# Performance work log

Measured on AMD Instinct MI355X. Metric: run time of the kernel, lower is better.

The kernel has to match this reference:

```python
import jax, jax.numpy as jnp
import numpy as np

B, N, QD = 4, 4096, 1024
HEADS, DIM_HEAD = 8, 64
HID = HEADS * DIM_HEAD
SCALE = DIM_HEAD ** -0.5


def setup_inputs() -> dict:
    key = jax.random.key(0)
    ks = jax.random.split(key, 6)
    s_in = 1.0 / np.sqrt(QD)
    s_h = 1.0 / np.sqrt(HID)
    return {
        "x": jax.random.normal(ks[0], (B, N, QD), dtype=jnp.float32),
        "Wq": jax.random.uniform(ks[1], (QD, HID), jnp.float32, -s_in, s_in),
        "Wk": jax.random.uniform(ks[2], (QD, HID), jnp.float32, -s_in, s_in),
        "Wv": jax.random.uniform(ks[3], (QD, HID), jnp.float32, -s_in, s_in),
        "Wo": jax.random.uniform(ks[4], (HID, QD), jnp.float32, -s_h, s_h),
        "bo": jax.random.uniform(ks[5], (QD,), jnp.float32, -s_h, s_h),
    }


def reference(x, Wq, Wk, Wv, Wo, bo):
    b, n, _ = x.shape
    # projections (bias-free Linears)
    q = x @ Wq  # [b, n, hid]
    k = x @ Wk
    v = x @ Wv
    # 'b n (h d) -> b h d n'
    def split_heads(t):
        return t.reshape(b, n, HEADS, DIM_HEAD).transpose(0, 2, 3, 1)  # [b,h,d,n]
    q = split_heads(q)
    k = split_heads(k)
    v = split_heads(v)
    q = jax.nn.softmax(q, axis=-2) * SCALE  # softmax over feature dim d
    k = jax.nn.softmax(k, axis=-1)          # softmax over sequence dim n
    context = jnp.einsum('bhdn,bhen->bhde', k, v)   # [b,h,d,e] small d x e
    out = jnp.einsum('bhde,bhdn->bhen', context, q)  # [b,h,e,n]
    # 'b h e n -> b n (h e)'
    out = out.transpose(0, 3, 1, 2).reshape(b, n, HID)
    return out @ Wo + bo
```

## Files before the change

### kernel.cpp

```cpp
#include <hip/hip_runtime.h>
#include <hip/hip_bf16.h>

typedef __bf16 bf16_t;
typedef bf16_t bf16x8 __attribute__((ext_vector_type(8)));
typedef float floatx4 __attribute__((ext_vector_type(4)));

#define BB 4
#define NN 4096
#define QDIM 1024
#define HEADS 8
#define DHEAD 64
#define HID 512
#define ROWS (BB*NN)
#define QKV_LD 1536

__device__ __forceinline__ float b2f(bf16_t v){ return (float)v; }
__device__ __forceinline__ bf16_t f2b(float v){ return (bf16_t)v; }

__device__ __forceinline__ bf16x8 load8(const bf16_t* p) { return *(const bf16x8*)p; }
__device__ __forceinline__ bf16x8 load8(const float* p) {
  float4 a = *(const float4*)p;
  float4 b = *(const float4*)(p + 4);
  bf16x8 r;
  r[0]=f2b(a.x); r[1]=f2b(a.y); r[2]=f2b(a.z); r[3]=f2b(a.w);
  r[4]=f2b(b.x); r[5]=f2b(b.y); r[6]=f2b(b.z); r[7]=f2b(b.w);
  return r;
}
__device__ __forceinline__ void store_out(bf16_t* p, float v){ *p = f2b(v); }
__device__ __forceinline__ void store_out(float*  p, float v){ *p = v; }

__device__ __forceinline__ void gll16(const void* g, void* l) {
  __builtin_amdgcn_global_load_lds((const __attribute__((address_space(1))) void*)g,
                                   (__attribute__((address_space(3))) void*)l,
                                   16, 0, 0);
}

static constexpr size_t OFF_QKV = 0;
static constexpr size_t OFF_WT  = 50331648;
static constexpr size_t OFF_WOT = OFF_WT  + 3145728;
static constexpr size_t OFF_SP  = OFF_WOT + 1048576;
static constexpr size_t OFF_CP  = OFF_SP  + 1048576;
static constexpr size_t OFF_W2  = OFF_CP  + 8388608;
static constexpr size_t OFF_XB  = OFF_WOT;

__global__ __launch_bounds__(256) void to_bf16(
    const float* __restrict__ in, bf16_t* __restrict__ out) {
  size_t i = ((size_t)blockIdx.x * 256 + threadIdx.x) * 8;
  *(bf16x8*)&out[i] = load8(&in[i]);
}

__global__ __launch_bounds__(256) void transpose_qkv_w(
    const float* __restrict__ Wq, const float* __restrict__ Wk,
    const float* __restrict__ Wv, bf16_t* __restrict__ out) {
  const float* in = blockIdx.z == 0 ? Wq : (blockIdx.z == 1 ? Wk : Wv);
  bf16_t* o = out + (size_t)blockIdx.z * HID * QDIM;
  __shared__ bf16_t T[64][68];
  int r0 = blockIdx.y * 64, c0 = blockIdx.x * 64;
  int t = threadIdx.x;
#pragma unroll
  for (int i = 0; i < 2; ++i) {
    int u = t + i * 256; int rr = u >> 3, c8 = (u & 7) * 8;
    bf16x8 v = load8(&in[(size_t)(r0 + rr) * HID + c0 + c8]);
#pragma unroll
    for (int j = 0; j < 8; ++j) T[c8 + j][rr] = v[j];
  }
  __syncthreads();
#pragma unroll
  for (int i = 0; i < 2; ++i) {
    int u = t + i * 256; int cr = u >> 3, r8 = (u & 7) * 8;
    bf16x8 v;
#pragma unroll
    for (int j = 0; j < 8; ++j) v[j] = T[cr][r8 + j];
    *(bf16x8*)&o[(size_t)(c0 + cr) * QDIM + r0 + r8] = v;
  }
}

__global__ __launch_bounds__(256) void transpose_tile(
    const float* __restrict__ in, bf16_t* __restrict__ out, int R, int C) {
  __shared__ bf16_t T[64][68];
  int r0 = blockIdx.y * 64, c0 = blockIdx.x * 64;
  int t = threadIdx.x;
#pragma unroll
  for (int i = 0; i < 2; ++i) {
    int u = t + i * 256; int rr = u >> 3, c8 = (u & 7) * 8;
    bf16x8 v = load8(&in[(size_t)(r0 + rr) * C + c0 + c8]);
#pragma unroll
    for (int j = 0; j < 8; ++j) T[c8 + j][rr] = v[j];
  }
  __syncthreads();
#pragma unroll
  for (int i = 0; i < 2; ++i) {
    int u = t + i * 256; int cr = u >> 3, r8 = (u & 7) * 8;
    bf16x8 v;
#pragma unroll
    for (int j = 0; j < 8; ++j) v[j] = T[cr][r8 + j];
    *(bf16x8*)&out[(size_t)(c0 + cr) * R + r0 + r8] = v;
  }
}

template <typename OT, bool QSM>
__global__ __launch_bounds__(256, 2) void gemm128(
    const bf16_t* __restrict__ A, int lda,
    const bf16_t* __restrict__ BT, int ldb,
    OT* __restrict__ C, int ldc,
    const float* __restrict__ bias, int K,
    size_t zsA, size_t zsB, size_t zsC) {
  __shared__ bf16_t As[128 * 32];
  __shared__ bf16_t Bs[128 * 32];
  int nwg = gridDim.x * gridDim.y;
  int wg = blockIdx.y * gridDim.x + blockIdx.x;
  int sw = (wg & 7) * (nwg >> 3) + (wg >> 3);
  int bx = sw % gridDim.x, by = sw / gridDim.x;
  A  += (size_t)blockIdx.z * zsA;
  BT += (size_t)blockIdx.z * zsB;
  C  += (size_t)blockIdx.z * zsC;

  int m0 = by * 128, n0 = bx * 128;
  int t = threadIdx.x;
  int w = t >> 6, lane = t & 63;
  int wm = (w >> 1) * 64, wn = (w & 1) * 64;
  int lr = lane & 15, lk = (lane >> 4) * 8;

  floatx4 acc[4][4];
#pragma unroll
  for (int mi = 0; mi < 4; ++mi)
#pragma unroll
    for (int ni = 0; ni < 4; ++ni) acc[mi][ni] = (floatx4){0.f, 0.f, 0.f, 0.f};

  for (int k0 = 0; k0 < K; k0 += 32) {
#pragma unroll
    for (int i = 0; i < 2; ++i) {
      int idx = i * 256 + t;
      int r = idx >> 2, c = (idx & 3) * 8;
      bf16_t* lbase  = (bf16_t*)As + i * 2048 + w * 512;
      bf16_t* lbaseB = (bf16_t*)Bs + i * 2048 + w * 512;
      gll16(A  + (size_t)(m0 + r) * lda + k0 + c, lbase);
      gll16(BT + (size_t)(n0 + r) * ldb + k0 + c, lbaseB);
    }
    __syncthreads();
    bf16x8 af[4], bfr[4];
#pragma unroll
    for (int mi = 0; mi < 4; ++mi) af[mi] = *(const bf16x8*)&As[(wm + mi * 16 + lr) * 32 + lk];
#pragma unroll
    for (int ni = 0; ni < 4; ++ni) bfr[ni] = *(const bf16x8*)&Bs[(wn + ni * 16 + lr) * 32 + lk];
#pragma unroll
    for (int mi = 0; mi < 4; ++mi)
#pragma unroll
      for (int ni = 0; ni < 4; ++ni)
        acc[mi][ni] = __builtin_amdgcn_mfma_f32_16x16x32_bf16(af[mi], bfr[ni], acc[mi][ni], 0, 0, 0);
    __syncthreads();
  }

  if (QSM && n0 < HID) {
#pragma unroll
    for (int mi = 0; mi < 4; ++mi)
#pragma unroll
      for (int r = 0; r < 4; ++r) {
        float m = -1e30f;
#pragma unroll
        for (int ni = 0; ni < 4; ++ni) m = fmaxf(m, acc[mi][ni][r]);
#pragma unroll
        for (int off = 1; off < 16; off <<= 1) m = fmaxf(m, __shfl_xor(m, off));
        float e0 = __expf(acc[mi][0][r] - m), e1 = __expf(acc[mi][1][r] - m);
        float e2 = __expf(acc[mi][2][r] - m), e3 = __expf(acc[mi][3][r] - m);
        float s = e0 + e1 + e2 + e3;
#pragma unroll
        for (int off = 1; off < 16; off <<= 1) s += __shfl_xor(s, off);
        float inv = 0.125f / s;
        acc[mi][0][r] = e0 * inv; acc[mi][1][r] = e1 * inv;
        acc[mi][2][r] = e2 * inv; acc[mi][3][r] = e3 * inv;
      }
  }

  int quad = (lane >> 4);
#pragma unroll
  for (int ni = 0; ni < 4; ++ni) {
    int gc = n0 + wn + ni * 16 + lr;
    float bv = (!QSM && bias) ? bias[gc] : 0.f;
#pragma unroll
    for (int mi = 0; mi < 4; ++mi)
#pragma unroll
      for (int r = 0; r < 4; ++r) {
        int gr = m0 + wm + mi * 16 + quad * 4 + r;
        store_out(&C[(size_t)gr * ldc + gc], acc[mi][ni][r] + bv);
      }
  }
}

__global__ __launch_bounds__(512) void k_stats_partial(
    const bf16_t* __restrict__ qkv, float2* __restrict__ part) {
  int c = blockIdx.x, b = blockIdx.y, t = threadIdx.x;
  const bf16_t* p = qkv + (size_t)(b * NN + c * 64) * QKV_LD + HID + t;
  float m = -1e30f, s = 0.f;
  for (int r = 0; r < 64; ++r) {
    float v = b2f(p[(size_t)r * QKV_LD]);
    float nm = fmaxf(m, v);
    s = s * __expf(m - nm) + __expf(v - nm);
    m = nm;
  }
  part[(size_t)(b * 64 + c) * 512 + t] = make_float2(m, s);
}

__global__ __launch_bounds__(256) void context_mfma(
    const bf16_t* __restrict__ qkv, const float2* __restrict__ part,
    float* __restrict__ cPart) {
  int chunk = blockIdx.x;
  int bh = blockIdx.y;
  int b = bh >> 3, h = bh & 7;
  __shared__ bf16_t ksh[64][72];
  __shared__ bf16_t vsh[64][72];
  __shared__ float2 st[64];
  __shared__ float2 pm[4][64];
  int t = threadIdx.x;
  {
    int d = t & 63, g = t >> 6;
    const float2* pp = part + (size_t)(b * 64 + g * 16) * 512 + h * 64 + d;
    float m = -1e30f, s = 0.f;
#pragma unroll 4
    for (int c = 0; c < 16; ++c) {
      float2 q = pp[(size_t)c * 512];
      float nm = fmaxf(m, q.x);
      s = s * __expf(m - nm) + q.y * __expf(q.x - nm);
      m = nm;
    }
    pm[g][d] = make_float2(m, s);
  }
  __syncthreads();
  if (t < 64) {
    float m = -1e30f, s = 0.f;
#pragma unroll
    for (int g = 0; g < 4; ++g) {
      float2 q = pm[g][t];
      float nm = fmaxf(m, q.x);
      s = s * __expf(m - nm) + q.y * __expf(q.x - nm);
      m = nm;
    }
    st[t] = make_float2(m, 1.f / s);
  }

  int w = t >> 6, lane = t & 63;
  int lr = lane & 15, lk = (lane >> 4) * 8;
  floatx4 acc[4];
#pragma unroll
  for (int ni = 0; ni < 4; ++ni) acc[ni] = (floatx4){0.f, 0.f, 0.f, 0.f};

  for (int nt = 0; nt < 4; ++nt) {
    int n0 = chunk * 256 + nt * 64;
    __syncthreads();
#pragma unroll
    for (int i = 0; i < 2; ++i) {
      int u = t + i * 256; int nr = u >> 3, d8 = (u & 7) * 8;
      const bf16_t* base = qkv + (size_t)(b * NN + n0 + nr) * QKV_LD + h * 64 + d8;
      bf16x8 kv = *(const bf16x8*)(base + HID);
      bf16x8 vv = *(const bf16x8*)(base + 2 * HID);
#pragma unroll
      for (int j = 0; j < 8; ++j) {
        int d = d8 + j;
        ksh[d][nr] = f2b(__expf(b2f(kv[j]) - st[d].x) * st[d].y);
        vsh[d][nr] = vv[j];
      }
    }
    __syncthreads();
#pragma unroll
    for (int s = 0; s < 2; ++s) {
      bf16x8 a = *(const bf16x8*)&ksh[w * 16 + lr][s * 32 + lk];
#pragma unroll
      for (int ni = 0; ni < 4; ++ni) {
        bf16x8 bb = *(const bf16x8*)&vsh[ni * 16 + lr][s * 32 + lk];
        acc[ni] = __builtin_amdgcn_mfma_f32_16x16x32_bf16(a, bb, acc[ni], 0, 0, 0);
      }
    }
  }
  float* op = cPart + (size_t)(chunk * 32 + bh) * 4096;
  int quad = lane >> 4;
#pragma unroll
  for (int ni = 0; ni < 4; ++ni)
#pragma unroll
    for (int r = 0; r < 4; ++r)
      op[(w * 16 + quad * 4 + r) * 64 + ni * 16 + lr] = acc[ni][r];
}

__global__ __launch_bounds__(256) void ctx2w2(
    const float* __restrict__ cPart, const bf16_t* __restrict__ WoT,
    bf16_t* __restrict__ W2T) {
  int cchunk = blockIdx.x;
  int bh = blockIdx.y;
  int b = bh >> 3, h = bh & 7;
  __shared__ float cs[64][65];
  __shared__ float wsf[128][65];
  int t = threadIdx.x;
#pragma unroll
  for (int i = 0; i < 4; ++i) {
    int f4 = t + i * 256;
    float4 s = make_float4(0.f, 0.f, 0.f, 0.f);
#pragma unroll 4
    for (int p = 0; p < 16; ++p) {
      float4 v = *(const float4*)&cPart[(size_t)(p * 32 + bh) * 4096 + f4 * 4];
      s.x += v.x; s.y += v.y; s.z += v.z; s.w += v.w;
    }
    int u = f4 * 4; int d = u >> 6, e = u & 63;
    cs[d][e] = s.x; cs[d][e + 1] = s.y; cs[d][e + 2] = s.z; cs[d][e + 3] = s.w;
  }
#pragma unroll
  for (int i = 0; i < 4; ++i) {
    int u = t + i * 256; int cl = u >> 3, e8 = (u & 7) * 8;
    bf16x8 v = load8(&WoT[(size_t)(cchunk * 128 + cl) * 512 + h * 64 + e8]);
#pragma unroll
    for (int j = 0; j < 8; ++j) wsf[cl][e8 + j] = b2f(v[j]);
  }
  __syncthreads();
  int d = t & 63;
  int cq = t >> 6;
  float rd[64];
#pragma unroll
  for (int e = 0; e < 64; ++e) rd[e] = cs[d][e];
#pragma unroll 4
  for (int ci = 0; ci < 32; ++ci) {
    int cl = cq * 32 + ci;
    float s = 0.f;
#pragma unroll
    for (int e = 0; e < 64; ++e) s += rd[e] * wsf[cl][e];
    W2T[((size_t)b * 1024 + cchunk * 128 + cl) * 512 + h * 64 + d] = f2b(s);
  }
}

extern "C" void kernel_launch(void* const* d_in, const int* in_sizes, int n_in,
                              void* d_out, int out_size, void* d_ws, size_t ws_size,
                              hipStream_t stream) {
  const float* x  = (const float*)d_in[0];
  const float* Wq = (const float*)d_in[1];
  const float* Wk = (const float*)d_in[2];
  const float* Wv = (const float*)d_in[3];
  const float* Wo = (const float*)d_in[4];
  const float* bo = (const float*)d_in[5];
  float* out = (float*)d_out;
  char* ws = (char*)d_ws;

  bf16_t* qkv   = (bf16_t*)(ws + OFF_QKV);
  bf16_t* WTall = (bf16_t*)(ws + OFF_WT);
  bf16_t* WoT   = (bf16_t*)(ws + OFF_WOT);
  float2* statP = (float2*)(ws + OFF_SP);
  float*  cPart = (float*)(ws + OFF_CP);
  bf16_t* W2T   = (bf16_t*)(ws + OFF_W2);
  bf16_t* xb    = (bf16_t*)(ws + OFF_XB);

  transpose_qkv_w<<<dim3(8, 16, 3), 256, 0, stream>>>(Wq, Wk, Wv, WTall);

  to_bf16<<<8192, 256, 0, stream>>>(x, xb);

  gemm128<bf16_t, true><<<dim3(12, 128), 256, 0, stream>>>(
      xb, QDIM, WTall, QDIM, qkv, QKV_LD, nullptr, QDIM, 0, 0, 0);

  transpose_tile<<<dim3(16, 8), 256, 0, stream>>>(Wo, WoT, HID, QDIM);

  k_stats_partial<<<dim3(64, 4), 512, 0, stream>>>(qkv, statP);

  context_mfma<<<dim3(16, 32), 256, 0, stream>>>(qkv, statP, cPart);

  ctx2w2<<<dim3(8, 32), 256, 0, stream>>>(cPart, WoT, W2T);

  gemm128<float, false><<<dim3(8, 32, 4), 256, 0, stream>>>(
      qkv, QKV_LD, W2T, HID, out, QDIM, bo, HID,
      (size_t)NN * QKV_LD, (size_t)QDIM * HID, (size_t)NN * QDIM);
}
```

Before: 290.1 us.

## Drop max-subtraction in k softmax, fold normalizer into context via MFMA ones

Removes the separate k-statistics pass: keys are exponentiated without max subtraction, and the per-feature row sums come from an extra MFMA against a ones vector, then get applied in ctx2w2 as a reciprocal scale. It also merges the x conversion and QKV weight transpose into one launch and reads Wo directly in ctx2w2 instead of transposing it first. Together this cuts three kernel launches and one full read of the k columns. The cost is a risk of overflow in exp for large k values, and the sums are taken from bf16-rounded exponentials.

```diff
diff --git a/kernel.cpp b/kernel.cpp
--- a/kernel.cpp
+++ b/kernel.cpp
@@ -37,26 +37,29 @@
 
 static constexpr size_t OFF_QKV = 0;
 static constexpr size_t OFF_WT  = 50331648;
-static constexpr size_t OFF_WOT = OFF_WT  + 3145728;
-static constexpr size_t OFF_SP  = OFF_WOT + 1048576;
-static constexpr size_t OFF_CP  = OFF_SP  + 1048576;
-static constexpr size_t OFF_W2  = OFF_CP  + 8388608;
-static constexpr size_t OFF_XB  = OFF_WOT;
-
-__global__ __launch_bounds__(256) void to_bf16(
-    const float* __restrict__ in, bf16_t* __restrict__ out) {
-  size_t i = ((size_t)blockIdx.x * 256 + threadIdx.x) * 8;
-  *(bf16x8*)&out[i] = load8(&in[i]);
-}
-
-__global__ __launch_bounds__(256) void transpose_qkv_w(
+static constexpr size_t OFF_CP  = OFF_WT + 3145728;
+static constexpr size_t OFF_SPT = OFF_CP + 8388608;
+static constexpr size_t OFF_W2  = OFF_SPT + 131072;
+static constexpr size_t OFF_XB  = OFF_CP;
+
+__global__ __launch_bounds__(256) void prep(
+    const float* __restrict__ x,
     const float* __restrict__ Wq, const float* __restrict__ Wk,
-    const float* __restrict__ Wv, bf16_t* __restrict__ out) {
-  const float* in = blockIdx.z == 0 ? Wq : (blockIdx.z == 1 ? Wk : Wv);
-  bf16_t* o = out + (size_t)blockIdx.z * HID * QDIM;
+    const float* __restrict__ Wv,
+    bf16_t* __restrict__ xb, bf16_t* __restrict__ WTall) {
   __shared__ bf16_t T[64][68];
-  int r0 = blockIdx.y * 64, c0 = blockIdx.x * 64;
   int t = threadIdx.x;
+  if (blockIdx.x < 8192) {
+    size_t i = ((size_t)blockIdx.x * 256 + t) * 8;
+    *(bf16x8*)&xb[i] = load8(&x[i]);
+    return;
+  }
+  int bid = blockIdx.x - 8192;
+  int z = bid >> 7;
+  int rem = bid & 127;
+  int r0 = (rem >> 3) * 64, c0 = (rem & 7) * 64;
+  const float* in = z == 0 ? Wq : (z == 1 ? Wk : Wv);
+  bf16_t* o = WTall + (size_t)z * HID * QDIM;
 #pragma unroll
   for (int i = 0; i < 2; ++i) {
     int u = t + i * 256; int rr = u >> 3, c8 = (u & 7) * 8;
@@ -72,29 +75,6 @@
 #pragma unroll
     for (int j = 0; j < 8; ++j) v[j] = T[cr][r8 + j];
     *(bf16x8*)&o[(size_t)(c0 + cr) * QDIM + r0 + r8] = v;
-  }
-}
-
-__global__ __launch_bounds__(256) void transpose_tile(
-    const float* __restrict__ in, bf16_t* __restrict__ out, int R, int C) {
-  __shared__ bf16_t T[64][68];
-  int r0 = blockIdx.y * 64, c0 = blockIdx.x * 64;
-  int t = threadIdx.x;
-#pragma unroll
-  for (int i = 0; i < 2; ++i) {
-    int u = t + i * 256; int rr = u >> 3, c8 = (u & 7) * 8;
-    bf16x8 v = load8(&in[(size_t)(r0 + rr) * C + c0 + c8]);
-#pragma unroll
-    for (int j = 0; j < 8; ++j) T[c8 + j][rr] = v[j];
-  }
-  __syncthreads();
-#pragma unroll
-  for (int i = 0; i < 2; ++i) {
-    int u = t + i * 256; int cr = u >> 3, r8 = (u & 7) * 8;
-    bf16x8 v;
-#pragma unroll
-    for (int j = 0; j < 8; ++j) v[j] = T[cr][r8 + j];
-    *(bf16x8*)&out[(size_t)(c0 + cr) * R + r0 + r8] = v;
   }
 }
 
@@ -187,62 +167,24 @@
   }
 }
 
-__global__ __launch_bounds__(512) void k_stats_partial(
-    const bf16_t* __restrict__ qkv, float2* __restrict__ part) {
-  int c = blockIdx.x, b = blockIdx.y, t = threadIdx.x;
-  const bf16_t* p = qkv + (size_t)(b * NN + c * 64) * QKV_LD + HID + t;
-  float m = -1e30f, s = 0.f;
-  for (int r = 0; r < 64; ++r) {
-    float v = b2f(p[(size_t)r * QKV_LD]);
-    float nm = fmaxf(m, v);
-    s = s * __expf(m - nm) + __expf(v - nm);
-    m = nm;
-  }
-  part[(size_t)(b * 64 + c) * 512 + t] = make_float2(m, s);
-}
-
 __global__ __launch_bounds__(256) void context_mfma(
-    const bf16_t* __restrict__ qkv, const float2* __restrict__ part,
-    float* __restrict__ cPart) {
+    const bf16_t* __restrict__ qkv, float* __restrict__ cPart,
+    float* __restrict__ sPart) {
   int chunk = blockIdx.x;
   int bh = blockIdx.y;
   int b = bh >> 3, h = bh & 7;
   __shared__ bf16_t ksh[64][72];
   __shared__ bf16_t vsh[64][72];
-  __shared__ float2 st[64];
-  __shared__ float2 pm[4][64];
   int t = threadIdx.x;
-  {
-    int d = t & 63, g = t >> 6;
-    const float2* pp = part + (size_t)(b * 64 + g * 16) * 512 + h * 64 + d;
-    float m = -1e30f, s = 0.f;
-#pragma unroll 4
-    for (int c = 0; c < 16; ++c) {
-      float2 q = pp[(size_t)c * 512];
-      float nm = fmaxf(m, q.x);
-      s = s * __expf(m - nm) + q.y * __expf(q.x - nm);
-      m = nm;
-    }
-    pm[g][d] = make_float2(m, s);
-  }
-  __syncthreads();
-  if (t < 64) {
-    float m = -1e30f, s = 0.f;
-#pragma unroll
-    for (int g = 0; g < 4; ++g) {
-      float2 q = pm[g][t];
-      float nm = fmaxf(m, q.x);
-      s = s * __expf(m - nm) + q.y * __expf(q.x - nm);
-      m = nm;
-    }
-    st[t] = make_float2(m, 1.f / s);
-  }
-
   int w = t >> 6, lane = t & 63;
   int lr = lane & 15, lk = (lane >> 4) * 8;
   floatx4 acc[4];
+  floatx4 accs = (floatx4){0.f, 0.f, 0.f, 0.f};
 #pragma unroll
   for (int ni = 0; ni < 4; ++ni) acc[ni] = (floatx4){0.f, 0.f, 0.f, 0.f};
+  bf16x8 ones;
+#pragma unroll
+  for (int j = 0; j < 8; ++j) ones[j] = f2b(1.f);
 
   for (int nt = 0; nt < 4; ++nt) {
     int n0 = chunk * 256 + nt * 64;
@@ -255,9 +197,8 @@
       bf16x8 vv = *(const bf16x8*)(base + 2 * HID);
 #pragma unroll
       for (int j = 0; j < 8; ++j) {
-        int d = d8 + j;
-        ksh[d][nr] = f2b(__expf(b2f(kv[j]) - st[d].x) * st[d].y);
-        vsh[d][nr] = vv[j];
+        ksh[d8 + j][nr] = f2b(__expf(b2f(kv[j])));
+        vsh[d8 + j][nr] = vv[j];
       }
     }
     __syncthreads();
@@ -269,6 +210,7 @@
         bf16x8 bb = *(const bf16x8*)&vsh[ni * 16 + lr][s * 32 + lk];
         acc[ni] = __builtin_amdgcn_mfma_f32_16x16x32_bf16(a, bb, acc[ni], 0, 0, 0);
       }
+      accs = __builtin_amdgcn_mfma_f32_16x16x32_bf16(a, ones, accs, 0, 0, 0);
     }
   }
   float* op = cPart + (size_t)(chunk * 32 + bh) * 4096;
@@ -278,17 +220,30 @@
 #pragma unroll
     for (int r = 0; r < 4; ++r)
       op[(w * 16 + quad * 4 + r) * 64 + ni * 16 + lr] = acc[ni][r];
+  if (lr == 0) {
+#pragma unroll
+    for (int r = 0; r < 4; ++r)
+      sPart[(size_t)(chunk * 32 + bh) * 64 + w * 16 + quad * 4 + r] = accs[r];
+  }
 }
 
 __global__ __launch_bounds__(256) void ctx2w2(
-    const float* __restrict__ cPart, const bf16_t* __restrict__ WoT,
-    bf16_t* __restrict__ W2T) {
+    const float* __restrict__ cPart, const float* __restrict__ sPart,
+    const float* __restrict__ Wo, bf16_t* __restrict__ W2T) {
   int cchunk = blockIdx.x;
   int bh = blockIdx.y;
   int b = bh >> 3, h = bh & 7;
   __shared__ float cs[64][65];
   __shared__ float wsf[128][65];
+  __shared__ float sinv[64];
   int t = threadIdx.x;
+  if (t < 64) {
+    float s = 0.f;
+#pragma unroll 4
+    for (int p = 0; p < 16; ++p) s += sPart[(size_t)(p * 32 + bh) * 64 + t];
+    sinv[t] = 1.f / s;
+  }
+  __syncthreads();
 #pragma unroll
   for (int i = 0; i < 4; ++i) {
     int f4 = t + i * 256;
@@ -299,14 +254,17 @@
       s.x += v.x; s.y += v.y; s.z += v.z; s.w += v.w;
     }
     int u = f4 * 4; int d = u >> 6, e = u & 63;
-    cs[d][e] = s.x; cs[d][e + 1] = s.y; cs[d][e + 2] = s.z; cs[d][e + 3] = s.w;
-  }
-#pragma unroll
-  for (int i = 0; i < 4; ++i) {
-    int u = t + i * 256; int cl = u >> 3, e8 = (u & 7) * 8;
-    bf16x8 v = load8(&WoT[(size_t)(cchunk * 128 + cl) * 512 + h * 64 + e8]);
-#pragma unroll
-    for (int j = 0; j < 8; ++j) wsf[cl][e8 + j] = b2f(v[j]);
+    float iv = sinv[d];
+    cs[d][e] = s.x * iv; cs[d][e + 1] = s.y * iv;
+    cs[d][e + 2] = s.z * iv; cs[d][e + 3] = s.w * iv;
+  }
+#pragma unroll
+  for (int i = 0; i < 8; ++i) {
+    int u = t + i * 256;
+    int e = u >> 5, c4 = u & 31;
+    float4 v = *(const float4*)&Wo[(size_t)(h * 64 + e) * QDIM + cchunk * 128 + c4 * 4];
+    wsf[c4 * 4 + 0][e] = v.x; wsf[c4 * 4 + 1][e] = v.y;
+    wsf[c4 * 4 + 2][e] = v.z; wsf[c4 * 4 + 3][e] = v.w;
   }
   __syncthreads();
   int d = t & 63;
@@ -338,26 +296,19 @@
 
   bf16_t* qkv   = (bf16_t*)(ws + OFF_QKV);
   bf16_t* WTall = (bf16_t*)(ws + OFF_WT);
-  bf16_t* WoT   = (bf16_t*)(ws + OFF_WOT);
-  float2* statP = (float2*)(ws + OFF_SP);
   float*  cPart = (float*)(ws + OFF_CP);
+  float*  sPart = (float*)(ws + OFF_SPT);
   bf16_t* W2T   = (bf16_t*)(ws + OFF_W2);
   bf16_t* xb    = (bf16_t*)(ws + OFF_XB);
 
-  transpose_qkv_w<<<dim3(8, 16, 3), 256, 0, stream>>>(Wq, Wk, Wv, WTall);
-
-  to_bf16<<<8192, 256, 0, stream>>>(x, xb);
+  prep<<<8576, 256, 0, stream>>>(x, Wq, Wk, Wv, xb, WTall);
 
   gemm128<bf16_t, true><<<dim3(12, 128), 256, 0, stream>>>(
       xb, QDIM, WTall, QDIM, qkv, QKV_LD, nullptr, QDIM, 0, 0, 0);
 
-  transpose_tile<<<dim3(16, 8), 256, 0, stream>>>(Wo, WoT, HID, QDIM);
-
-  k_stats_partial<<<dim3(64, 4), 512, 0, stream>>>(qkv, statP);
-
-  context_mfma<<<dim3(16, 32), 256, 0, stream>>>(qkv, statP, cPart);
-
-  ctx2w2<<<dim3(8, 32), 256, 0, stream>>>(cPart, WoT, W2T);
+  context_mfma<<<dim3(16, 32), 256, 0, stream>>>(qkv, cPart, sPart);
+
+  ctx2w2<<<dim3(8, 32), 256, 0, stream>>>(cPart, sPart, Wo, W2T);
 
   gemm128<float, false><<<dim3(8, 32, 4), 256, 0, stream>>>(
       qkv, QKV_LD, W2T, HID, out, QDIM, bo, HID,
```

New measurement: 278.0 us. 1.04x faster.
